# Kernel optimization log

Hardware: AMD Instinct MI355X
Metric: run time of the kernel (lower is better)

The kernel has to match this reference:

```python
import jax, jax.numpy as jnp
import numpy as np

N = 30000
F_IN = 500
HID = 16
OUT = 3
E = 960000


def setup_inputs() -> dict:
    key = jax.random.key(0)
    ks = jax.random.split(key, 10)
    x = jax.random.normal(ks[0], (N, F_IN), dtype=jnp.float32)
    edge_index = jax.random.randint(ks[1], (2, E), 0, N, dtype=jnp.int32)
    # CNN params (torch Conv1d: weight [out, in, k], bias [out])
    s1 = 1.0 / np.sqrt(1 * 3)
    s2 = 1.0 / np.sqrt(HID * 3)
    conv1_w = jax.random.uniform(ks[2], (HID, 1, 3), jnp.float32, -s1, s1)
    conv1_b = jax.random.uniform(ks[3], (HID,), jnp.float32, -s1, s1)
    conv2_w = jax.random.uniform(ks[4], (HID, HID, 3), jnp.float32, -s2, s2)
    conv2_b = jax.random.uniform(ks[5], (HID,), jnp.float32, -s2, s2)
    # GCNConv params (glorot weight [in, out], zero bias)
    g1 = np.sqrt(6.0 / (HID + HID))
    g2 = np.sqrt(6.0 / (HID + OUT))
    gcn1_w = jax.random.uniform(ks[6], (HID, HID), jnp.float32, -g1, g1)
    gcn1_b = jnp.zeros((HID,), jnp.float32)
    gcn2_w = jax.random.uniform(ks[7], (HID, OUT), jnp.float32, -g2, g2)
    gcn2_b = jnp.zeros((OUT,), jnp.float32)
    return {"x": x, "conv1_w": conv1_w, "conv1_b": conv1_b,
            "conv2_w": conv2_w, "conv2_b": conv2_b,
            "gcn1_w": gcn1_w, "gcn1_b": gcn1_b,
            "gcn2_w": gcn2_w, "gcn2_b": gcn2_b,
            "edge_index": edge_index}


def _conv1d(x, w, b):
    # x: [N, C_in, L], w: [C_out, C_in, 3], padding=1
    y = jax.lax.conv_general_dilated(
        x, w, window_strides=(1,), padding=[(1, 1)],
        dimension_numbers=("NCH", "OIH", "NCH"))
    return y + b[None, :, None]


def _gcn_conv(x, w, b, src, dst, n):
    # x: [n, d_in] -> [n, d_out]; Kipf normalization with self-loops
    h = x @ w
    loop = jnp.arange(n, dtype=src.dtype)
    s = jnp.concatenate([src, loop])
    d = jnp.concatenate([dst, loop])
    deg = jax.ops.segment_sum(jnp.ones_like(d, dtype=h.dtype), d, num_segments=n)
    dinv = jnp.where(deg > 0, jax.lax.rsqrt(deg), 0.0)
    norm = dinv[s] * dinv[d]                      # [E+n]
    msg = h[s] * norm[:, None]                    # gather + scale
    return jax.ops.segment_sum(msg, d, num_segments=n) + b


def reference(x, conv1_w, conv1_b, conv2_w, conv2_b,
              gcn1_w, gcn1_b, gcn2_w, gcn2_b, edge_index):
    # CNN feature extractor over feature axis
    h = x[:, None, :]                             # [N, 1, F_IN]
    h = jax.nn.relu(_conv1d(h, conv1_w, conv1_b))  # [N, HID, F_IN]
    h = jax.nn.relu(_conv1d(h, conv2_w, conv2_b))  # [N, HID, F_IN]
    h = jnp.max(h, axis=2)                        # global max pool -> [N, HID]
    # GCN
    src, dst = edge_index[0], edge_index[1]
    n = h.shape[0]
    h = jax.nn.relu(_gcn_conv(h, gcn1_w, gcn1_b, src, dst, n))
    h = _gcn_conv(h, gcn2_w, gcn2_b, src, dst, n)  # [N, OUT]
    return jax.nn.log_softmax(h, axis=1)
```

## Files before the change

### kernel.cpp

```cpp
#include <hip/hip_runtime.h>
#include <hip/hip_bf16.h>

#define N_NODES 30000
#define F_INLEN 500
#define HID 16
#define OUTC 3
#define NEDGE 960000
#define YPITCH 20
#define NBIN 938
#define HBLK 256
#define EPRH (NEDGE / HBLK)
#define ECAP 1536
#define NPB2 118

typedef float  f32x4 __attribute__((ext_vector_type(4)));
typedef float  f32x2 __attribute__((ext_vector_type(2)));
typedef short  s16x8 __attribute__((ext_vector_type(8)));

static __device__ __forceinline__ unsigned short f2bf(float f) {
    unsigned int u = __float_as_uint(f);
    unsigned int r = (u + 0x7fffu + ((u >> 16) & 1u)) >> 16;
    return (unsigned short)r;
}
static __device__ __forceinline__ unsigned int pack_bf16x2(float v0, float v1) {
#if __has_builtin(__builtin_amdgcn_cvt_pk_bf16_f32)
    typedef __bf16 bf16x2_t __attribute__((ext_vector_type(2)));
    union { bf16x2_t v; unsigned int u; } cv;
    cv.v = __builtin_amdgcn_cvt_pk_bf16_f32(v0, v1);
    return cv.u;
#else
    return __builtin_amdgcn_perm(__float_as_uint(v1), __float_as_uint(v0), 0x07060302);
#endif
}

__global__ void setup_kernel(const float* __restrict__ w2, short* __restrict__ bfragsG,
                             int* __restrict__ degi)
{
    const int tid = threadIdx.x;
    const int gid = blockIdx.x * 256 + tid;
    if (gid < N_NODES) degi[gid] = 0;
    if (blockIdx.x == 0 && tid < 64) {
        const int n16 = tid & 15, q = tid >> 4;
#pragma unroll
        for (int j = 0; j < 8; j++) {
            {
                const int c = q * 8 + j;
                const int t = c >> 4, i = c & 15;
                bfragsG[tid * 16 + j] = (short)f2bf(w2[n16 * 48 + i * 3 + t]);
            }
            {
                const int c = 32 + q * 8 + j;
                short v = 0;
                if (c < 48) { const int t = c >> 4, i = c & 15; v = (short)f2bf(w2[n16 * 48 + i * 3 + t]); }
                bfragsG[tid * 16 + 8 + j] = v;
            }
        }
    }
}

__global__ __launch_bounds__(256, 7) void conv_hist(
    const float* __restrict__ x,
    const float* __restrict__ w1, const float* __restrict__ b1,
    const float* __restrict__ b2, const short* __restrict__ bfragsG,
    const int* __restrict__ dst, int* __restrict__ degi,
    int* __restrict__ cntbase, float* __restrict__ h0)
{
    __shared__ __align__(16) float xp[502];
    __shared__ __align__(16) unsigned short yh[516 * YPITCH];
    __shared__ float red[64];

    const int tid = threadIdx.x;

    if (blockIdx.x < HBLK) {
        int* histH = (int*)yh;
        for (int i = tid; i < NBIN; i += 256) histH[i] = 0;
        __syncthreads();
        const int e0 = blockIdx.x * EPRH;
        for (int e = e0 + tid; e < e0 + EPRH; e += 256) {
            const int d = dst[e];
            atomicAdd(&histH[d >> 5], 1);
            atomicAdd(&degi[d], 1);
        }
        __syncthreads();
        for (int i = tid; i < NBIN; i += 256) cntbase[i * HBLK + blockIdx.x] = histH[i];
        return;
    }

    const int node = blockIdx.x - HBLK;
    const int lane = tid & 63;
    const int wave = tid >> 6;
    const int n16  = lane & 15;
    const int q    = lane >> 4;

    if (tid == 0) { xp[0] = 0.f; xp[501] = 0.f; }
    if (tid < 125) {
        const float4 v = ((const float4*)(x + (long long)node * F_INLEN))[tid];
        xp[4 * tid + 1] = v.x; xp[4 * tid + 2] = v.y;
        xp[4 * tid + 3] = v.z; xp[4 * tid + 4] = v.w;
    }
    {
        const int ri = tid >> 4;
        const int row = (ri == 0) ? 0 : (500 + ri);
        yh[row * YPITCH + (tid & 15)] = 0;
    }
    const s16x8* bfp = (const s16x8*)(bfragsG + lane * 16);
    const s16x8 bh0 = bfp[0], bh1 = bfp[1];

    f32x2 wt0[8], wt1[8], wt2[8], bb[8];
#pragma unroll
    for (int cp = 0; cp < 8; cp++) {
        const int c0 = 2 * cp, c1 = 2 * cp + 1;
        wt0[cp] = (f32x2){w1[c0 * 3 + 0], w1[c1 * 3 + 0]};
        wt1[cp] = (f32x2){w1[c0 * 3 + 1], w1[c1 * 3 + 1]};
        wt2[cp] = (f32x2){w1[c0 * 3 + 2], w1[c1 * 3 + 2]};
        bb[cp]  = (f32x2){b1[c0], b1[c1]};
    }
    __syncthreads();

    for (int p = tid; p < 500; p += 256) {
        const float x0 = xp[p], x1 = xp[p + 1], x2 = xp[p + 2];
        const f32x2 xv0 = {x0, x0}, xv1 = {x1, x1}, xv2 = {x2, x2};
        const f32x2 zero = {0.f, 0.f};
        unsigned int hp[8];
#pragma unroll
        for (int cp = 0; cp < 8; cp++) {
            f32x2 a = bb[cp];
            a = __builtin_elementwise_fma(wt0[cp], xv0, a);
            a = __builtin_elementwise_fma(wt1[cp], xv1, a);
            a = __builtin_elementwise_fma(wt2[cp], xv2, a);
            a = __builtin_elementwise_max(a, zero);
            hp[cp] = pack_bf16x2(a[0], a[1]);
        }
        uint2* d = (uint2*)&yh[(p + 1) * YPITCH];
        d[0] = make_uint2(hp[0], hp[1]);
        d[1] = make_uint2(hp[2], hp[3]);
        d[2] = make_uint2(hp[4], hp[5]);
        d[3] = make_uint2(hp[6], hp[7]);
    }
    __syncthreads();

    struct S8 { short4 lo, hi; };
    float mx0 = -3.0e38f, mx1 = -3.0e38f, mx2 = -3.0e38f, mx3 = -3.0e38f;
#pragma unroll
    for (int it = 0; it < 8; it++) {
        const int tile = wave * 8 + it;
        const int p0 = tile * 16 + n16;
        const int cA = (q & 1) * 8;
        const int rA = p0 + (q >> 1);
        const int rB = p0 + 2 + (q >> 1);
        S8 t0, t1;
        t0.lo = *(const short4*)&yh[rA * YPITCH + cA];
        t0.hi = *(const short4*)&yh[rA * YPITCH + cA + 4];
        t1.lo = *(const short4*)&yh[rB * YPITCH + cA];
        t1.hi = *(const short4*)&yh[rB * YPITCH + cA + 4];
        const s16x8 ah0 = *(const s16x8*)&t0;
        const s16x8 ah1 = *(const s16x8*)&t1;
        f32x4 acc = {0.f, 0.f, 0.f, 0.f};
        acc = __builtin_amdgcn_mfma_f32_16x16x32_bf16(ah0, bh0, acc, 0, 0, 0);
        acc = __builtin_amdgcn_mfma_f32_16x16x32_bf16(ah1, bh1, acc, 0, 0, 0);
        if (it < 7) {
            mx0 = fmaxf(mx0, acc[0]);
            mx1 = fmaxf(mx1, acc[1]);
            mx2 = fmaxf(mx2, acc[2]);
            mx3 = fmaxf(mx3, acc[3]);
        } else if (wave < 3) {
            mx0 = fmaxf(mx0, acc[0]);
            mx1 = fmaxf(mx1, acc[1]);
            mx2 = fmaxf(mx2, acc[2]);
            mx3 = fmaxf(mx3, acc[3]);
        } else if (q == 0) {
            mx0 = fmaxf(mx0, acc[0]);
            mx1 = fmaxf(mx1, acc[1]);
            mx2 = fmaxf(mx2, acc[2]);
            mx3 = fmaxf(mx3, acc[3]);
        }
    }
    float m = fmaxf(fmaxf(mx0, mx1), fmaxf(mx2, mx3));
    m = fmaxf(m, __shfl_xor(m, 16));
    m = fmaxf(m, __shfl_xor(m, 32));
    if (lane < 16) red[wave * 16 + lane] = m;
    __syncthreads();
    if (tid < 16) {
        const float mm = fmaxf(fmaxf(red[tid], red[16 + tid]), fmaxf(red[32 + tid], red[48 + tid]));
        h0[node * HID + tid] = fmaxf(mm + b2[tid], 0.f);
    }
}

__global__ __launch_bounds__(512) void reorder2(
    const int* __restrict__ src, const int* __restrict__ dst,
    const int* __restrict__ cntbase, int* __restrict__ packed,
    int* __restrict__ binstart, const int* __restrict__ degi,
    float* __restrict__ dinv, float* __restrict__ h0)
{
    __shared__ int scA[NBIN], scB[NBIN];
    __shared__ int gexc[NBIN];
    __shared__ int lexc[NBIN];
    __shared__ int cursor[NBIN];
    __shared__ int srt[EPRH];
    const int tid = threadIdx.x;
    const int blk = blockIdx.x;

    const int kblk = blk >> 2, rem = blk & 3;
    for (int bin = tid; bin < NBIN; bin += 512) {
        const int4* row = (const int4*)(cntbase + bin * HBLK);
        int tot = 0, psum = 0, lc = 0;
        for (int k = 0; k < kblk; k++) {
            const int4 v = row[k];
            const int s4 = v.x + v.y + v.z + v.w;
            tot += s4; psum += s4;
        }
        {
            const int4 v = row[kblk];
            tot += v.x + v.y + v.z + v.w;
            if (rem > 0) psum += v.x;
            if (rem > 1) psum += v.y;
            if (rem > 2) psum += v.z;
            lc = (rem == 0) ? v.x : (rem == 1) ? v.y : (rem == 2) ? v.z : v.w;
        }
        for (int k = kblk + 1; k < HBLK / 4; k++) {
            const int4 v = row[k];
            tot += v.x + v.y + v.z + v.w;
        }
        cursor[bin] = tot;
        gexc[bin]   = psum;
        lexc[bin]   = lc;
        scA[bin]    = tot;
    }
    __syncthreads();
    {
        int* pA = scA; int* pB = scB;
        for (int off = 1; off < NBIN; off <<= 1) {
            for (int i = tid; i < NBIN; i += 512)
                pB[i] = pA[i] + ((i >= off) ? pA[i - off] : 0);
            __syncthreads();
            int* tp = pA; pA = pB; pB = tp;
        }
        for (int i = tid; i < NBIN; i += 512) {
            const int excl = pA[i] - cursor[i];
            gexc[i] += excl;
            if (blk == 0) binstart[i] = excl;
        }
        if (blk == 0 && tid == 0) binstart[NBIN] = NEDGE;
    }
    __syncthreads();
    for (int i = tid; i < NBIN; i += 512) scA[i] = lexc[i];
    __syncthreads();
    {
        int* pA = scA; int* pB = scB;
        for (int off = 1; off < NBIN; off <<= 1) {
            for (int i = tid; i < NBIN; i += 512)
                pB[i] = pA[i] + ((i >= off) ? pA[i - off] : 0);
            __syncthreads();
            int* tp = pA; pA = pB; pB = tp;
        }
        for (int i = tid; i < NBIN; i += 512) {
            const int e2 = pA[i] - lexc[i];
            lexc[i] = e2;
            cursor[i] = e2;
        }
    }
    __syncthreads();
    const int e0 = blk * EPRH;
    for (int e = e0 + tid; e < e0 + EPRH; e += 512) {
        const int d = dst[e];
        const int bin = d >> 5;
        const int pos = atomicAdd(&cursor[bin], 1);
        srt[pos] = src[e] | (d << 15);
    }
    __syncthreads();
    for (int i = tid; i < EPRH; i += 512) {
        const int bin = srt[i] >> 20;
        packed[gexc[bin] + (i - lexc[bin])] = srt[i];
    }
    const int n0 = blk * NPB2;
    for (int n = n0 + tid; n < n0 + NPB2 && n < N_NODES; n += 512) {
        const float dv = rsqrtf((float)(degi[n] + 1));
        dinv[n] = dv;
        f32x4* h4 = (f32x4*)(h0 + n * HID);
#pragma unroll
        for (int k = 0; k < 4; k++) h4[k] = h4[k] * dv;
    }
}

__global__ __launch_bounds__(256) void agg1_kernel(
    const int* __restrict__ binstart, const int* __restrict__ packed,
    const float* __restrict__ h0, const float* __restrict__ dinv,
    const float* __restrict__ W1, const float* __restrict__ b1g,
    const float* __restrict__ W2, float4* __restrict__ t2p4)
{
    __shared__ float w1s[256];
    __shared__ float w2s[48];
    __shared__ float b1s[16];
    __shared__ float accS[32 * 17];
    __shared__ int eL[ECAP];
    __shared__ int srt[ECAP];
    __shared__ int h32[32], ls32[32], lofs32[32];
    const int tid = threadIdx.x;
    const int blk = blockIdx.x;
    w1s[tid] = W1[tid];
    if (tid < 48) w2s[tid] = W2[tid];
    if (tid < 16) b1s[tid] = b1g[tid];
    if (tid < 32) h32[tid] = 0;
    const int beg = binstart[blk];
    const int cnt = binstart[blk + 1] - beg;
    __syncthreads();
    for (int j = tid; j < cnt; j += 256) {
        const int p = packed[beg + j];
        eL[j] = p;
        atomicAdd(&h32[(p >> 15) & 31], 1);
    }
    __syncthreads();
    if (tid < 32) {
        const int v = h32[tid];
        int inc = v;
#pragma unroll
        for (int off = 1; off < 32; off <<= 1) {
            const int y = __shfl_up(inc, off);
            if (tid >= off) inc += y;
        }
        ls32[tid] = inc - v;
        lofs32[tid] = inc - v;
    }
    __syncthreads();
    for (int j = tid; j < cnt; j += 256) {
        const int p = eL[j];
        const int pos = atomicAdd(&lofs32[(p >> 15) & 31], 1);
        srt[pos] = p;
    }
    __syncthreads();
    const int n = tid >> 3;
    const int eslot = (tid >> 2) & 1;
    const int q = tid & 3;
    const int node = blk * 32 + n;
    const bool valid = node < N_NODES;
    f32x4 acc = {0.f, 0.f, 0.f, 0.f};
    if (valid) {
        const int s0 = ls32[n];
        const int s1 = s0 + h32[n];
        for (int i = s0 + eslot; i < s1; i += 2) {
            const int s = srt[i] & 32767;
            acc += *(const f32x4*)(h0 + s * HID + q * 4);
        }
    }
#pragma unroll
    for (int c = 0; c < 4; c++) acc[c] += __shfl_xor(acc[c], 4);
    if (valid && eslot == 0) {
        acc += *(const f32x4*)(h0 + node * HID + q * 4);
        accS[n * 17 + q * 4 + 0] = acc[0];
        accS[n * 17 + q * 4 + 1] = acc[1];
        accS[n * 17 + q * 4 + 2] = acc[2];
        accS[n * 17 + q * 4 + 3] = acc[3];
    }
    __syncthreads();
    if (tid < 128) {
        const int n2 = tid >> 2;
        const int node2 = blk * 32 + n2;
        if (node2 < N_NODES) {
            const float dv = dinv[node2];
            const int q2 = tid & 3;
            float y0 = 0.f, y1 = 0.f, y2 = 0.f, y3 = 0.f;
#pragma unroll
            for (int i = 0; i < 16; i++) {
                const float a = accS[n2 * 17 + i];
                y0 = fmaf(a, w1s[i * 16 + q2 * 4 + 0], y0);
                y1 = fmaf(a, w1s[i * 16 + q2 * 4 + 1], y1);
                y2 = fmaf(a, w1s[i * 16 + q2 * 4 + 2], y2);
                y3 = fmaf(a, w1s[i * 16 + q2 * 4 + 3], y3);
            }
            float d0 = 0.f, d1 = 0.f, d2 = 0.f;
            const float yv[4] = {y0, y1, y2, y3};
#pragma unroll
            for (int j = 0; j < 4; j++) {
                const int o = q2 * 4 + j;
                const float h = fmaxf(b1s[o] + dv * yv[j], 0.f);
                d0 = fmaf(h, w2s[o * 3 + 0], d0);
                d1 = fmaf(h, w2s[o * 3 + 1], d1);
                d2 = fmaf(h, w2s[o * 3 + 2], d2);
            }
            d0 += __shfl_xor(d0, 1); d0 += __shfl_xor(d0, 2);
            d1 += __shfl_xor(d1, 1); d1 += __shfl_xor(d1, 2);
            d2 += __shfl_xor(d2, 1); d2 += __shfl_xor(d2, 2);
            if (q2 == 0) t2p4[node2] = make_float4(d0 * dv, d1 * dv, d2 * dv, 0.f);
        }
    }
}

__global__ __launch_bounds__(256) void agg2_kernel(
    const int* __restrict__ binstart, const int* __restrict__ packed,
    const float4* __restrict__ t2p4, const float* __restrict__ dinv,
    const float* __restrict__ b2g, float* __restrict__ out)
{
    __shared__ int eL[ECAP];
    __shared__ int srt[ECAP];
    __shared__ int h32[32], ls32[32], lofs32[32];
    const int tid = threadIdx.x;
    const int blk = blockIdx.x;
    if (tid < 32) h32[tid] = 0;
    const int beg = binstart[blk];
    const int cnt = binstart[blk + 1] - beg;
    __syncthreads();
    for (int j = tid; j < cnt; j += 256) {
        const int p = packed[beg + j];
        eL[j] = p;
        atomicAdd(&h32[(p >> 15) & 31], 1);
    }
    __syncthreads();
    if (tid < 32) {
        const int v = h32[tid];
        int inc = v;
#pragma unroll
        for (int off = 1; off < 32; off <<= 1) {
            const int y = __shfl_up(inc, off);
            if (tid >= off) inc += y;
        }
        ls32[tid] = inc - v;
        lofs32[tid] = inc - v;
    }
    __syncthreads();
    for (int j = tid; j < cnt; j += 256) {
        const int p = eL[j];
        const int pos = atomicAdd(&lofs32[(p >> 15) & 31], 1);
        srt[pos] = p;
    }
    __syncthreads();
    const int n = tid >> 3;
    const int ln8 = tid & 7;
    const int node = blk * 32 + n;
    float a0 = 0.f, a1 = 0.f, a2 = 0.f;
    if (node < N_NODES) {
        const int s0 = ls32[n];
        const int s1 = s0 + h32[n];
        for (int i = s0 + ln8; i < s1; i += 8) {
            const int s = srt[i] & 32767;
            const float4 v = t2p4[s];
            a0 += v.x; a1 += v.y; a2 += v.z;
        }
    }
#pragma unroll
    for (int msk = 1; msk < 8; msk <<= 1) {
        a0 += __shfl_xor(a0, msk);
        a1 += __shfl_xor(a1, msk);
        a2 += __shfl_xor(a2, msk);
    }
    if (ln8 == 0 && node < N_NODES) {
        const float dv = dinv[node];
        const float4 self = t2p4[node];
        const float z0 = b2g[0] + dv * (a0 + self.x);
        const float z1 = b2g[1] + dv * (a1 + self.y);
        const float z2 = b2g[2] + dv * (a2 + self.z);
        const float m = fmaxf(z0, fmaxf(z1, z2));
        const float lg = m + logf(expf(z0 - m) + expf(z1 - m) + expf(z2 - m));
        out[node * 3 + 0] = z0 - lg;
        out[node * 3 + 1] = z1 - lg;
        out[node * 3 + 2] = z2 - lg;
    }
}

extern "C" void kernel_launch(void* const* d_in, const int* in_sizes, int n_in,
                              void* d_out, int out_size, void* d_ws, size_t ws_size,
                              hipStream_t stream)
{
    const float* x   = (const float*)d_in[0];
    const float* w1  = (const float*)d_in[1];
    const float* b1  = (const float*)d_in[2];
    const float* w2  = (const float*)d_in[3];
    const float* b2  = (const float*)d_in[4];
    const float* g1w = (const float*)d_in[5];
    const float* g1b = (const float*)d_in[6];
    const float* g2w = (const float*)d_in[7];
    const float* g2b = (const float*)d_in[8];
    const int*   ei  = (const int*)d_in[9];
    const int* src = ei;
    const int* dst = ei + NEDGE;

    float* ws = (float*)d_ws;
    float*  h0      = ws;
    float*  dinv    = ws + 480000;
    float4* t2p4    = (float4*)(ws + 510000);
    int*    degi    = (int*)(ws + 630000);
    int*    cntbase = (int*)(ws + 660000);
    int*    binstart= (int*)(ws + 900128);
    int*    packed  = (int*)(ws + 901152);
    short*  bfragsG = (short*)(ws + 1861152);
    float*  out     = (float*)d_out;

    setup_kernel<<<118, 256, 0, stream>>>(w2, bfragsG, degi);
    conv_hist<<<HBLK + N_NODES, 256, 0, stream>>>(x, w1, b1, b2, bfragsG,
                                                  dst, degi, cntbase, h0);
    reorder2<<<HBLK, 512, 0, stream>>>(src, dst, cntbase, packed, binstart,
                                       degi, dinv, h0);
    agg1_kernel<<<NBIN, 256, 0, stream>>>(binstart, packed, h0, dinv,
                                          g1w, g1b, g2w, t2p4);
    agg2_kernel<<<NBIN, 256, 0, stream>>>(binstart, packed, t2p4, dinv, g2b, out);
}
```

Measured before the change: 266.0 us.

## Halve histogram blocks, transpose count layout, recompute dinv from bin counts

Halves the number of histogram/reorder blocks, so each reorder block sorts twice as many edges in shared memory. The per-block bin counts are now stored block-major, and reorder sums them with a coalesced scalar loop over blocks instead of int4 row reads. The aggregation kernels compute the degree normalization from the per-node edge counts they already hold in shared memory, rather than loading dinv from global memory. Fewer blocks means less parallelism in the histogram and reorder phases but less count data to scan.

Measured after the change: 226.5 us. 1.17x faster.

```diff
diff --git a/kernel.cpp b/kernel.cpp
--- a/kernel.cpp
+++ b/kernel.cpp
@@ -8,10 +8,10 @@
 #define NEDGE 960000
 #define YPITCH 20
 #define NBIN 938
-#define HBLK 256
+#define HBLK 128
 #define EPRH (NEDGE / HBLK)
 #define ECAP 1536
-#define NPB2 118
+#define NPB2 235
 
 typedef float  f32x4 __attribute__((ext_vector_type(4)));
 typedef float  f32x2 __attribute__((ext_vector_type(2)));
@@ -82,7 +82,7 @@
             atomicAdd(&degi[d], 1);
         }
         __syncthreads();
-        for (int i = tid; i < NBIN; i += 256) cntbase[i * HBLK + blockIdx.x] = histH[i];
+        for (int i = tid; i < NBIN; i += 256) cntbase[blockIdx.x * NBIN + i] = histH[i];
         return;
     }
 
@@ -200,26 +200,13 @@
     const int tid = threadIdx.x;
     const int blk = blockIdx.x;
 
-    const int kblk = blk >> 2, rem = blk & 3;
     for (int bin = tid; bin < NBIN; bin += 512) {
-        const int4* row = (const int4*)(cntbase + bin * HBLK);
         int tot = 0, psum = 0, lc = 0;
-        for (int k = 0; k < kblk; k++) {
-            const int4 v = row[k];
-            const int s4 = v.x + v.y + v.z + v.w;
-            tot += s4; psum += s4;
-        }
-        {
-            const int4 v = row[kblk];
-            tot += v.x + v.y + v.z + v.w;
-            if (rem > 0) psum += v.x;
-            if (rem > 1) psum += v.y;
-            if (rem > 2) psum += v.z;
-            lc = (rem == 0) ? v.x : (rem == 1) ? v.y : (rem == 2) ? v.z : v.w;
-        }
-        for (int k = kblk + 1; k < HBLK / 4; k++) {
-            const int4 v = row[k];
-            tot += v.x + v.y + v.z + v.w;
+        for (int k = 0; k < HBLK; k++) {
+            const int c = cntbase[k * NBIN + bin];
+            tot += c;
+            if (k < blk) psum += c;
+            if (k == blk) lc = c;
         }
         cursor[bin] = tot;
         gexc[bin]   = psum;
@@ -284,7 +271,7 @@
 
 __global__ __launch_bounds__(256) void agg1_kernel(
     const int* __restrict__ binstart, const int* __restrict__ packed,
-    const float* __restrict__ h0, const float* __restrict__ dinv,
+    const float* __restrict__ h0,
     const float* __restrict__ W1, const float* __restrict__ b1g,
     const float* __restrict__ W2, float4* __restrict__ t2p4)
 {
@@ -356,7 +343,7 @@
         const int n2 = tid >> 2;
         const int node2 = blk * 32 + n2;
         if (node2 < N_NODES) {
-            const float dv = dinv[node2];
+            const float dv = rsqrtf((float)(h32[n2] + 1));
             const int q2 = tid & 3;
             float y0 = 0.f, y1 = 0.f, y2 = 0.f, y3 = 0.f;
 #pragma unroll
@@ -387,7 +374,7 @@
 
 __global__ __launch_bounds__(256) void agg2_kernel(
     const int* __restrict__ binstart, const int* __restrict__ packed,
-    const float4* __restrict__ t2p4, const float* __restrict__ dinv,
+    const float4* __restrict__ t2p4,
     const float* __restrict__ b2g, float* __restrict__ out)
 {
     __shared__ int eL[ECAP];
@@ -443,7 +430,7 @@
         a2 += __shfl_xor(a2, msk);
     }
     if (ln8 == 0 && node < N_NODES) {
-        const float dv = dinv[node];
+        const float dv = rsqrtf((float)(h32[n] + 1));
         const float4 self = t2p4[node];
         const float z0 = b2g[0] + dv * (a0 + self.x);
         const float z1 = b2g[1] + dv * (a1 + self.y);
@@ -479,9 +466,9 @@
     float4* t2p4    = (float4*)(ws + 510000);
     int*    degi    = (int*)(ws + 630000);
     int*    cntbase = (int*)(ws + 660000);
-    int*    binstart= (int*)(ws + 900128);
-    int*    packed  = (int*)(ws + 901152);
-    short*  bfragsG = (short*)(ws + 1861152);
+    int*    binstart= (int*)(ws + 780064);
+    int*    packed  = (int*)(ws + 781024);
+    short*  bfragsG = (short*)(ws + 1741024);
     float*  out     = (float*)d_out;
 
     setup_kernel<<<118, 256, 0, stream>>>(w2, bfragsG, degi);
@@ -489,7 +476,7 @@
                                                   dst, degi, cntbase, h0);
     reorder2<<<HBLK, 512, 0, stream>>>(src, dst, cntbase, packed, binstart,
                                        degi, dinv, h0);
-    agg1_kernel<<<NBIN, 256, 0, stream>>>(binstart, packed, h0, dinv,
+    agg1_kernel<<<NBIN, 256, 0, stream>>>(binstart, packed, h0,
                                           g1w, g1b, g2w, t2p4);
-    agg2_kernel<<<NBIN, 256, 0, stream>>>(binstart, packed, t2p4, dinv, g2b, out);
-}
+    agg2_kernel<<<NBIN, 256, 0, stream>>>(binstart, packed, t2p4, g2b, out);
+}
```
